# Kernel optimization log

Measured on AMD Instinct MI355X. Metric: run time of the kernel, lower is better.

## Reference

```python
import jax, jax.numpy as jnp
import numpy as np

H = 768
NH = 12
HD = H // NH  # 64


def setup_inputs() -> dict:
    key = jax.random.key(0)
    ks = jax.random.split(key, 10)
    B, S = 8, 1024
    x = jax.random.normal(ks[0], (B, S, H), dtype=jnp.float32)
    attention_mask = jax.random.randint(ks[1], (B, S), 0, 2, dtype=jnp.int32)
    s = 1.0 / np.sqrt(H)
    Wq = jax.random.normal(ks[2], (H, H), jnp.float32) * s
    bq = jnp.zeros((H,), jnp.float32)
    Wk = jax.random.normal(ks[3], (H, H), jnp.float32) * s
    bk = jnp.zeros((H,), jnp.float32)
    Wv = jax.random.normal(ks[4], (H, H), jnp.float32) * s
    bv = jnp.zeros((H,), jnp.float32)
    Wo = jax.random.normal(ks[5], (H, H), jnp.float32) * s
    bo = jnp.zeros((H,), jnp.float32)
    return {"x": x, "attention_mask": attention_mask,
            "Wq": Wq, "bq": bq, "Wk": Wk, "bk": bk,
            "Wv": Wv, "bv": bv, "Wo": Wo, "bo": bo}


def reference(x, attention_mask, Wq, bq, Wk, bk, Wv, bv, Wo, bo):
    B, S, _ = x.shape
    scale = HD ** -0.5
    # projections -> [B, NH, S, HD]
    def split_heads(t):
        return t.reshape(B, S, NH, HD).transpose(0, 2, 1, 3)
    q = split_heads(x @ Wq.T + bq)
    k = split_heads(x @ Wk.T + bk)
    v = split_heads(x @ Wv.T + bv)
    scores = jnp.einsum('bhqd,bhkd->bhqk', q, k) * scale  # [B,NH,S,S]
    mask = attention_mask[:, None, None, :]  # [B,1,1,S]
    scores = jnp.where(mask == 0, jnp.float32(-10000.0), scores)
    probs = jax.nn.softmax(scores, axis=-1)
    ctx = jnp.einsum('bhqk,bhkd->bhqd', probs, v)  # [B,NH,S,HD]
    ctx = ctx.transpose(0, 2, 1, 3).reshape(B, S, H)
    out = ctx @ Wo.T + bo
    return out
```

## Files before the change

### kernel.cpp

```cpp
#include <hip/hip_runtime.h>
#include <hip/hip_bf16.h>

#define HDIM 768
#define NH 12
#define HD 64
#define BB 8
#define SS 1024
#define MROWS (BB*SS)
#define NQKV (3*HDIM)
#define GK 768
#define NHALF (GK/32)

#define SCL2E 0.18033688011f
#define MASKNEG -14426.9504f

typedef __attribute__((ext_vector_type(8))) short bf16x8;
typedef __attribute__((ext_vector_type(4))) float f32x4;

__device__ __forceinline__ unsigned short f2bf(float f) {
    unsigned int u = __float_as_uint(f);
    unsigned int r = (u + 0x7fffu + ((u >> 16) & 1u)) >> 16;
    return (unsigned short)r;
}

__device__ __forceinline__ void gload_lds16(const void* gsrc, void* ldst) {
    __builtin_amdgcn_global_load_lds(
        (const __attribute__((address_space(1))) unsigned int*)gsrc,
        (__attribute__((address_space(3))) unsigned int*)ldst,
        16, 0, 0);
}

__global__ void pack_all(const float* __restrict__ x,
                         const float* __restrict__ Wq, const float* __restrict__ Wk,
                         const float* __restrict__ Wv, const float* __restrict__ Wo,
                         const float* __restrict__ bq, const float* __restrict__ bk,
                         const float* __restrict__ bv, const int* __restrict__ m,
                         unsigned short* __restrict__ xb, unsigned short* __restrict__ wqkv,
                         unsigned short* __restrict__ wo,
                         float* __restrict__ biasq, float* __restrict__ madd)
{
    const int tid = blockIdx.x * blockDim.x + threadIdx.x;
    const int stride = gridDim.x * blockDim.x;
    for (int i = tid; i < 2162688; i += stride) {
        const float* src; unsigned short* dst; int off;
        if (i < 1572864) { src = x; dst = xb; off = i; }
        else {
            int j = i - 1572864;
            int seg = j / 147456;
            off = j - seg * 147456;
            src = (seg == 0) ? Wq : (seg == 1) ? Wk : (seg == 2) ? Wv : Wo;
            dst = (seg == 3) ? wo : wqkv + seg * (HDIM * HDIM);
        }
        float4 v = reinterpret_cast<const float4*>(src)[off];
        union { unsigned short u[4]; unsigned long long q; } o;
        o.u[0] = f2bf(v.x); o.u[1] = f2bf(v.y); o.u[2] = f2bf(v.z); o.u[3] = f2bf(v.w);
        reinterpret_cast<unsigned long long*>(dst)[off] = o.q;
    }
    if (tid < 3 * HDIM)
        biasq[tid] = (tid < HDIM) ? bq[tid] : (tid < 2 * HDIM) ? bk[tid - HDIM] : bv[tid - 2 * HDIM];
    if (tid < BB * SS)
        madd[tid] = (m[tid] == 0) ? MASKNEG : 0.0f;
}

template<int MODE>
__global__ __launch_bounds__(256)
void gemm_bt(const unsigned short* __restrict__ A,
             const unsigned short* __restrict__ Bw,
             const float* __restrict__ bias,
             unsigned short* __restrict__ qb,
             unsigned short* __restrict__ kb,
             unsigned short* __restrict__ vtb,
             float* __restrict__ fout,
             int gridN)
{
    __shared__ unsigned short As[4][128 * 32];
    __shared__ unsigned short Bs[4][128 * 32];
    const int tid  = threadIdx.x;
    const int wave = tid >> 6;
    const int lane = tid & 63;

    const int nwg = gridDim.x;
    const int cpx = nwg >> 3;
    const int wg  = (blockIdx.x & 7) * cpx + (blockIdx.x >> 3);
    const int bm = (wg / gridN) * 128;
    const int bn = (wg % gridN) * 128;

    const int wm = (wave >> 1) * 64;
    const int wn = (wave & 1) * 64;
    const int lr  = lane & 15;
    const int hv  = lane >> 4;
    const int rsw = (lr >> 1) & 3;
    const int srow = lane >> 2;
    const int sslot = lane & 3;
    const int skg = sslot ^ ((srow >> 1) & 3);

    f32x4 zero4 = {0.f, 0.f, 0.f, 0.f};
    f32x4 acc[4][4];
#pragma unroll
    for (int i = 0; i < 4; i++)
#pragma unroll
        for (int j = 0; j < 4; j++) acc[i][j] = zero4;

    auto stage = [&](int h) {
        const int slot = h & 3;
        const int k0 = h * 32;
#pragma unroll
        for (int j = 0; j < 2; ++j) {
            int rbase = (wave * 2 + j) * 16;
            int row = rbase + srow;
            gload_lds16(A  + (size_t)(bm + row) * GK + k0 + skg * 8, &As[slot][rbase * 32]);
            gload_lds16(Bw + (size_t)(bn + row) * GK + k0 + skg * 8, &Bs[slot][rbase * 32]);
        }
    };

    stage(0); stage(1); stage(2);

#pragma unroll
    for (int h = 0; h < NHALF; ++h) {
        const int rem = NHALF - 1 - h;
        if (rem >= 2)      { asm volatile("s_waitcnt vmcnt(8)" ::: "memory"); }
        else if (rem == 1) { asm volatile("s_waitcnt vmcnt(4)" ::: "memory"); }
        else               { asm volatile("s_waitcnt vmcnt(0)" ::: "memory"); }
        __builtin_amdgcn_s_barrier();
        __builtin_amdgcn_sched_barrier(0);

        if (h + 3 < NHALF) stage(h + 3);

        const int slot = h & 3;
        bf16x8 af[4], bf[4];
#pragma unroll
        for (int mi = 0; mi < 4; mi++)
            af[mi] = *(const bf16x8*)&As[slot][(wm + mi * 16 + lr) * 32 + ((hv ^ rsw) * 8)];
#pragma unroll
        for (int ni = 0; ni < 4; ni++)
            bf[ni] = *(const bf16x8*)&Bs[slot][(wn + ni * 16 + lr) * 32 + ((hv ^ rsw) * 8)];

        __builtin_amdgcn_s_setprio(1);
#pragma unroll
        for (int mi = 0; mi < 4; mi++)
#pragma unroll
            for (int ni = 0; ni < 4; ni++)
                acc[mi][ni] = __builtin_amdgcn_mfma_f32_16x16x32_bf16(
                    af[mi], bf[ni], acc[mi][ni], 0, 0, 0);
        __builtin_amdgcn_s_setprio(0);
    }

    const int rgrp = lane >> 4;
#pragma unroll
    for (int mi = 0; mi < 4; mi++)
#pragma unroll
        for (int ni = 0; ni < 4; ni++)
#pragma unroll
            for (int r = 0; r < 4; r++) {
                int m = bm + wm + mi * 16 + rgrp * 4 + r;
                int n = bn + wn + ni * 16 + lr;
                float v = acc[mi][ni][r] + bias[n];
                if (MODE == 0) {
                    int which = n / HDIM;
                    int nn = n - which * HDIM;
                    int h = nn >> 6, d = nn & 63;
                    int b = m >> 10, s = m & 1023;
                    unsigned short bvv = f2bf(v);
                    if (which == 0)      qb [(((size_t)(b * NH + h)) * SS + s) * HD + d] = bvv;
                    else if (which == 1) kb [(((size_t)(b * NH + h)) * SS + s) * HD + d] = bvv;
                    else                 vtb[(((size_t)(b * NH + h)) * HD + d) * SS + s] = bvv;
                } else {
                    fout[(size_t)m * HDIM + n] = v;
                }
            }
}

__global__ __launch_bounds__(256, 4)
void attn_kernel(const unsigned short* __restrict__ qb,
                 const unsigned short* __restrict__ kb,
                 const unsigned short* __restrict__ vtb,
                 const float* __restrict__ maskadd,
                 unsigned short* __restrict__ ctx)
{
    __shared__ unsigned short Ks[64][64];
    __shared__ unsigned short Vs[64][64];
    __shared__ unsigned short Ps[4][16][64];

    const int tid  = threadIdx.x;
    const int wave = tid >> 6;
    const int lane = tid & 63;
    const int wg = (blockIdx.x & 7) * 192 + (blockIdx.x >> 3);
    const int qt = wg & 15;
    const int h  = (wg >> 4) % NH;
    const int b  = wg / 192;
    const int bh = b * NH + h;
    const int q0 = qt * 64 + wave * 16;
    const int lr  = lane & 15;
    const int hi  = lane >> 4;
    const int e3  = lr & 7;
    const int srow = lane >> 3;
    const int sg   = lane & 7;

    const unsigned short* Qp = qb  + (size_t)bh * SS * HD;
    const unsigned short* Kp = kb  + (size_t)bh * SS * HD;
    const unsigned short* Vp = vtb + (size_t)bh * HD * SS;
    const float* madd = maskadd + b * SS;

    bf16x8 aq[2];
#pragma unroll
    for (int kk = 0; kk < 2; kk++)
        aq[kk] = *(const bf16x8*)&Qp[(size_t)(q0 + lr) * HD + kk * 32 + hi * 8];

    f32x4 zero4 = {0.f, 0.f, 0.f, 0.f};
    f32x4 o[4];
#pragma unroll
    for (int i = 0; i < 4; i++) o[i] = zero4;
    float plsum = 0.f;

    bf16x8 kreg[2], vreg[2];
    auto ld = [&](int t0) {
#pragma unroll
        for (int jj = 0; jj < 2; ++jj) {
            int rr = (wave * 2 + jj) * 8 + srow;
            kreg[jj] = *(const bf16x8*)&Kp[(size_t)(t0 + rr) * HD + sg * 8];
            vreg[jj] = *(const bf16x8*)&Vp[(size_t)rr * SS + t0 + sg * 8];
        }
    };
    auto wr = [&]() {
        const int slot = (sg ^ srow) * 8;
#pragma unroll
        for (int jj = 0; jj < 2; ++jj) {
            int rr = (wave * 2 + jj) * 8 + srow;
            *(bf16x8*)&Ks[rr][slot] = kreg[jj];
            *(bf16x8*)&Vs[rr][slot] = vreg[jj];
        }
    };

    ld(0);
    wr();
    __syncthreads();

    for (int t0 = 0; t0 < SS; t0 += 64) {
        const bool more = (t0 + 64 < SS);
        if (more) ld(t0 + 64);

        f32x4 sacc[4];
#pragma unroll
        for (int ni = 0; ni < 4; ni++) sacc[ni] = zero4;
        __builtin_amdgcn_s_setprio(1);
#pragma unroll
        for (int kk = 0; kk < 2; kk++)
#pragma unroll
            for (int ni = 0; ni < 4; ni++) {
                bf16x8 kf = *(const bf16x8*)&Ks[ni * 16 + lr][((kk * 4 + hi) ^ e3) * 8];
                sacc[ni] = __builtin_amdgcn_mfma_f32_16x16x32_bf16(kf, aq[kk], sacc[ni], 0, 0, 0);
            }
        __builtin_amdgcn_s_setprio(0);

        float4 md[4];
#pragma unroll
        for (int ni = 0; ni < 4; ni++)
            md[ni] = *(const float4*)&madd[t0 + ni * 16 + hi * 4];

        float p[4][4];
#pragma unroll
        for (int ni = 0; ni < 4; ni++) {
            p[ni][0] = __builtin_amdgcn_exp2f(fmaf(sacc[ni][0], SCL2E, md[ni].x));
            p[ni][1] = __builtin_amdgcn_exp2f(fmaf(sacc[ni][1], SCL2E, md[ni].y));
            p[ni][2] = __builtin_amdgcn_exp2f(fmaf(sacc[ni][2], SCL2E, md[ni].z));
            p[ni][3] = __builtin_amdgcn_exp2f(fmaf(sacc[ni][3], SCL2E, md[ni].w));
            plsum += p[ni][0] + p[ni][1] + p[ni][2] + p[ni][3];
        }

#pragma unroll
        for (int ni = 0; ni < 4; ni++) {
            union { __hip_bfloat162 h2[2]; unsigned long long q; } u;
            u.h2[0] = __float22bfloat162_rn(make_float2(p[ni][0], p[ni][1]));
            u.h2[1] = __float22bfloat162_rn(make_float2(p[ni][2], p[ni][3]));
            *(unsigned long long*)&Ps[wave][lr][((4 * ni + hi) ^ (e3 << 1)) * 4] = u.q;
        }

        __builtin_amdgcn_s_setprio(1);
#pragma unroll
        for (int ks = 0; ks < 2; ks++) {
            bf16x8 pa = *(const bf16x8*)&Ps[wave][lr][((8 * ks + 2 * hi) ^ (e3 << 1)) * 4];
#pragma unroll
            for (int nd = 0; nd < 4; nd++) {
                bf16x8 vb = *(const bf16x8*)&Vs[nd * 16 + lr][((4 * ks + hi) ^ e3) * 8];
                o[nd] = __builtin_amdgcn_mfma_f32_16x16x32_bf16(pa, vb, o[nd], 0, 0, 0);
            }
        }
        __builtin_amdgcn_s_setprio(0);

        __syncthreads();
        if (more) {
            wr();
            __syncthreads();
        }
    }

    float lrun = plsum;
    lrun += __shfl_xor(lrun, 16);
    lrun += __shfl_xor(lrun, 32);
    float iv[4];
#pragma unroll
    for (int r = 0; r < 4; r++) iv[r] = 1.0f / __shfl(lrun, hi * 4 + r, 16);
#pragma unroll
    for (int r = 0; r < 4; r++) {
        int grow = b * SS + qt * 64 + wave * 16 + hi * 4 + r;
#pragma unroll
        for (int nd = 0; nd < 4; nd++)
            ctx[(size_t)grow * HDIM + h * HD + nd * 16 + lr] = f2bf(o[nd][r] * iv[r]);
    }
}

extern "C" void kernel_launch(void* const* d_in, const int* in_sizes, int n_in,
                              void* d_out, int out_size, void* d_ws, size_t ws_size,
                              hipStream_t stream)
{
    const float* x    = (const float*)d_in[0];
    const int*   amask= (const int*)d_in[1];
    const float* Wq   = (const float*)d_in[2];
    const float* bq   = (const float*)d_in[3];
    const float* Wk   = (const float*)d_in[4];
    const float* bk   = (const float*)d_in[5];
    const float* Wv   = (const float*)d_in[6];
    const float* bv   = (const float*)d_in[7];
    const float* Wo   = (const float*)d_in[8];
    const float* bo   = (const float*)d_in[9];
    float* out = (float*)d_out;

    char* ws = (char*)d_ws;
    unsigned short* xb   = (unsigned short*)(ws);
    unsigned short* wqkv = (unsigned short*)(ws + 12582912);
    unsigned short* wo   = (unsigned short*)(ws + 16121856);
    float*          biasq= (float*)(ws + 17301504);
    unsigned short* qb   = (unsigned short*)(ws + 17310720);
    unsigned short* kb   = (unsigned short*)(ws + 29893632);
    unsigned short* vtb  = (unsigned short*)(ws + 42476544);
    unsigned short* ctx  = (unsigned short*)(ws + 55059456);
    float*          madd = (float*)(ws + 67642368);

    pack_all<<<2048, 256, 0, stream>>>(x, Wq, Wk, Wv, Wo, bq, bk, bv, amask,
                                       xb, wqkv, wo, biasq, madd);

    gemm_bt<0><<<(MROWS / 128) * (NQKV / 128), 256, 0, stream>>>(
        xb, wqkv, biasq, qb, kb, vtb, nullptr, NQKV / 128);

    attn_kernel<<<(SS / 64) * NH * BB, 256, 0, stream>>>(qb, kb, vtb, madd, ctx);

    gemm_bt<1><<<(MROWS / 128) * (HDIM / 128), 256, 0, stream>>>(
        ctx, wo, bo, nullptr, nullptr, nullptr, out, HDIM / 128);
}
```

Baseline: 147.1 us.

## Replace 128x128 GEMM with 256x256-tile, 8-wave, double-buffered LDS GEMM

Both projection GEMMs move from a 128x128 tile with 4 waves and a 4-slot ring buffer to a 256x256 tile with 8 waves and 128 KB of dynamic LDS. K advances 64 at a time, split into two 32-wide halves, with double buffering. A and B loads for the next steps are interleaved between MFMA groups, separated by barriers. The larger tile raises arithmetic intensity and cuts global traffic per FLOP. The cost is far fewer workgroups (288 for QKV, only 96 for the output projection on a 256-CU part), likely one workgroup per CU because of the LDS size, and possible tail and underutilization effects.

```diff
diff --git a/kernel.cpp b/kernel.cpp
--- a/kernel.cpp
+++ b/kernel.cpp
@@ -9,7 +9,7 @@
 #define MROWS (BB*SS)
 #define NQKV (3*HDIM)
 #define GK 768
-#define NHALF (GK/32)
+#define NT 12
 
 #define SCL2E 0.18033688011f
 #define MASKNEG -14426.9504f
@@ -63,8 +63,8 @@
 }
 
 template<int MODE>
-__global__ __launch_bounds__(256)
-void gemm_bt(const unsigned short* __restrict__ A,
+__global__ __launch_bounds__(512, 2)
+void gemm256(const unsigned short* __restrict__ A,
              const unsigned short* __restrict__ Bw,
              const float* __restrict__ bias,
              unsigned short* __restrict__ qb,
@@ -73,8 +73,7 @@
              float* __restrict__ fout,
              int gridN)
 {
-    __shared__ unsigned short As[4][128 * 32];
-    __shared__ unsigned short Bs[4][128 * 32];
+    extern __shared__ unsigned short lds[];
     const int tid  = threadIdx.x;
     const int wave = tid >> 6;
     const int lane = tid & 63;
@@ -82,78 +81,103 @@
     const int nwg = gridDim.x;
     const int cpx = nwg >> 3;
     const int wg  = (blockIdx.x & 7) * cpx + (blockIdx.x >> 3);
-    const int bm = (wg / gridN) * 128;
-    const int bn = (wg % gridN) * 128;
-
-    const int wm = (wave >> 1) * 64;
-    const int wn = (wave & 1) * 64;
-    const int lr  = lane & 15;
-    const int hv  = lane >> 4;
-    const int rsw = (lr >> 1) & 3;
-    const int srow = lane >> 2;
-    const int sslot = lane & 3;
-    const int skg = sslot ^ ((srow >> 1) & 3);
-
+    const int bm = (wg / gridN) * 256;
+    const int bn = (wg % gridN) * 256;
+
+    const int wr = wave >> 2;
+    const int wc = wave & 3;
+    const int lr = lane & 15;
+    const int hv = lane >> 4;
+    const int sl = (hv ^ ((lr >> 1) & 3)) * 8;
+
+    const int strow = tid >> 2;
+    const int stslot = tid & 3;
+
+#define ASP(buf,kh) (lds + (((buf) * 2 + (kh)) * 8192))
+#define BSP(buf,kh) (lds + 32768 + (((buf) * 2 + (kh)) * 8192))
+
+    f32x4 acc[8][4];
     f32x4 zero4 = {0.f, 0.f, 0.f, 0.f};
-    f32x4 acc[4][4];
-#pragma unroll
-    for (int i = 0; i < 4; i++)
+#pragma unroll
+    for (int i = 0; i < 8; i++)
 #pragma unroll
         for (int j = 0; j < 4; j++) acc[i][j] = zero4;
 
-    auto stage = [&](int h) {
-        const int slot = h & 3;
-        const int k0 = h * 32;
+    auto stageU = [&](const unsigned short* __restrict__ src, int rowbase,
+                      unsigned short* dst, int T, int kh) {
 #pragma unroll
         for (int j = 0; j < 2; ++j) {
-            int rbase = (wave * 2 + j) * 16;
-            int row = rbase + srow;
-            gload_lds16(A  + (size_t)(bm + row) * GK + k0 + skg * 8, &As[slot][rbase * 32]);
-            gload_lds16(Bw + (size_t)(bn + row) * GK + k0 + skg * 8, &Bs[slot][rbase * 32]);
+            int row = j * 128 + strow;
+            int g = stslot ^ ((row >> 1) & 3);
+            gload_lds16(src + (size_t)(rowbase + row) * GK + T * 64 + kh * 32 + g * 8,
+                        dst + j * 4096 + wave * 512);
         }
     };
 
-    stage(0); stage(1); stage(2);
-
-#pragma unroll
-    for (int h = 0; h < NHALF; ++h) {
-        const int rem = NHALF - 1 - h;
-        if (rem >= 2)      { asm volatile("s_waitcnt vmcnt(8)" ::: "memory"); }
-        else if (rem == 1) { asm volatile("s_waitcnt vmcnt(4)" ::: "memory"); }
-        else               { asm volatile("s_waitcnt vmcnt(0)" ::: "memory"); }
+    bf16x8 bfr[4];
+
+    auto mfma16 = [&](const unsigned short* Abase, int hmi) {
+        bf16x8 afr[4];
+#pragma unroll
+        for (int i = 0; i < 4; i++)
+            afr[i] = *(const bf16x8*)&Abase[(wr * 128 + (hmi * 4 + i) * 16 + lr) * 32 + sl];
+        __builtin_amdgcn_s_setprio(1);
+#pragma unroll
+        for (int i = 0; i < 4; i++)
+#pragma unroll
+            for (int ni = 0; ni < 4; ni++)
+                acc[hmi * 4 + i][ni] = __builtin_amdgcn_mfma_f32_16x16x32_bf16(
+                    afr[i], bfr[ni], acc[hmi * 4 + i][ni], 0, 0, 0);
+        __builtin_amdgcn_s_setprio(0);
+    };
+
+    stageU(A,  bm, ASP(0,0), 0, 0);
+    stageU(Bw, bn, BSP(0,0), 0, 0);
+    stageU(A,  bm, ASP(0,1), 0, 1);
+    stageU(Bw, bn, BSP(0,1), 0, 1);
+    stageU(A,  bm, ASP(1,0), 1, 0);
+    stageU(Bw, bn, BSP(1,0), 1, 0);
+
+#pragma unroll
+    for (int T = 0; T < NT; ++T) {
+        const int buf = T & 1;
+        if (T <= 10) { asm volatile("s_waitcnt vmcnt(8)" ::: "memory"); }
+        else         { asm volatile("s_waitcnt vmcnt(4)" ::: "memory"); }
         __builtin_amdgcn_s_barrier();
         __builtin_amdgcn_sched_barrier(0);
-
-        if (h + 3 < NHALF) stage(h + 3);
-
-        const int slot = h & 3;
-        bf16x8 af[4], bf[4];
-#pragma unroll
-        for (int mi = 0; mi < 4; mi++)
-            af[mi] = *(const bf16x8*)&As[slot][(wm + mi * 16 + lr) * 32 + ((hv ^ rsw) * 8)];
 #pragma unroll
         for (int ni = 0; ni < 4; ni++)
-            bf[ni] = *(const bf16x8*)&Bs[slot][(wn + ni * 16 + lr) * 32 + ((hv ^ rsw) * 8)];
-
-        __builtin_amdgcn_s_setprio(1);
-#pragma unroll
-        for (int mi = 0; mi < 4; mi++)
-#pragma unroll
-            for (int ni = 0; ni < 4; ni++)
-                acc[mi][ni] = __builtin_amdgcn_mfma_f32_16x16x32_bf16(
-                    af[mi], bf[ni], acc[mi][ni], 0, 0, 0);
-        __builtin_amdgcn_s_setprio(0);
+            bfr[ni] = *(const bf16x8*)&BSP(buf,0)[(wc * 64 + ni * 16 + lr) * 32 + sl];
+        if (T + 1 < NT) stageU(A, bm, ASP(1 - buf, 1), T + 1, 1);
+        mfma16(ASP(buf,0), 0);
+        __builtin_amdgcn_s_barrier();
+        __builtin_amdgcn_sched_barrier(0);
+        if (T + 1 < NT) stageU(Bw, bn, BSP(1 - buf, 1), T + 1, 1);
+        mfma16(ASP(buf,0), 1);
+        if (T <= 10) { asm volatile("s_waitcnt vmcnt(8)" ::: "memory"); }
+        else         { asm volatile("s_waitcnt vmcnt(0)" ::: "memory"); }
+        __builtin_amdgcn_s_barrier();
+        __builtin_amdgcn_sched_barrier(0);
+#pragma unroll
+        for (int ni = 0; ni < 4; ni++)
+            bfr[ni] = *(const bf16x8*)&BSP(buf,1)[(wc * 64 + ni * 16 + lr) * 32 + sl];
+        if (T + 2 < NT) stageU(A, bm, ASP(buf, 0), T + 2, 0);
+        mfma16(ASP(buf,1), 0);
+        __builtin_amdgcn_s_barrier();
+        __builtin_amdgcn_sched_barrier(0);
+        if (T + 2 < NT) stageU(Bw, bn, BSP(buf, 0), T + 2, 0);
+        mfma16(ASP(buf,1), 1);
     }
 
     const int rgrp = lane >> 4;
 #pragma unroll
-    for (int mi = 0; mi < 4; mi++)
+    for (int mi = 0; mi < 8; mi++)
 #pragma unroll
         for (int ni = 0; ni < 4; ni++)
 #pragma unroll
             for (int r = 0; r < 4; r++) {
-                int m = bm + wm + mi * 16 + rgrp * 4 + r;
-                int n = bn + wn + ni * 16 + lr;
+                int m = bm + wr * 128 + mi * 16 + rgrp * 4 + r;
+                int n = bn + wc * 64 + ni * 16 + lr;
                 float v = acc[mi][ni][r] + bias[n];
                 if (MODE == 0) {
                     int which = n / HDIM;
@@ -168,6 +192,8 @@
                     fout[(size_t)m * HDIM + n] = v;
                 }
             }
+#undef ASP
+#undef BSP
 }
 
 __global__ __launch_bounds__(256, 4)
@@ -336,14 +362,19 @@
     unsigned short* ctx  = (unsigned short*)(ws + 55059456);
     float*          madd = (float*)(ws + 67642368);
 
+    hipFuncSetAttribute((const void*)gemm256<0>,
+                        hipFuncAttributeMaxDynamicSharedMemorySize, 131072);
+    hipFuncSetAttribute((const void*)gemm256<1>,
+                        hipFuncAttributeMaxDynamicSharedMemorySize, 131072);
+
     pack_all<<<2048, 256, 0, stream>>>(x, Wq, Wk, Wv, Wo, bq, bk, bv, amask,
                                        xb, wqkv, wo, biasq, madd);
 
-    gemm_bt<0><<<(MROWS / 128) * (NQKV / 128), 256, 0, stream>>>(
-        xb, wqkv, biasq, qb, kb, vtb, nullptr, NQKV / 128);
+    gemm256<0><<<(MROWS / 256) * (NQKV / 256), 512, 131072, stream>>>(
+        xb, wqkv, biasq, qb, kb, vtb, nullptr, NQKV / 256);
 
     attn_kernel<<<(SS / 64) * NH * BB, 256, 0, stream>>>(qb, kb, vtb, madd, ctx);
 
-    gemm_bt<1><<<(MROWS / 128) * (HDIM / 128), 256, 0, stream>>>(
-        ctx, wo, bo, nullptr, nullptr, nullptr, out, HDIM / 128);
-}
+    gemm256<1><<<(MROWS / 256) * (HDIM / 256), 512, 131072, stream>>>(
+        ctx, wo, bo, nullptr, nullptr, nullptr, out, HDIM / 256);
+}
```

Result: slower. 165.0 us (+12.1%).
